# Optimization experiments

Hardware: AMD Instinct MI355X
Metric: run time of the kernel (lower is better)

Reference implementation:

```python
import jax, jax.numpy as jnp
import numpy as np

B, S, D, H = 32, 1024, 256, 256


def setup_inputs() -> dict:
    key = jax.random.key(0)
    ks = jax.random.split(key, 7)
    s_in = 1.0 / np.sqrt(D)
    s_h = 1.0 / np.sqrt(H)
    x = jax.random.normal(ks[0], (B, S, D), dtype=jnp.float32)
    # gate order: i, f, g, o stacked along last dim -> 4H
    W_fwd = jax.random.uniform(ks[1], (D, 4 * H), dtype=jnp.float32, minval=-s_in, maxval=s_in)
    U_fwd = jax.random.uniform(ks[2], (H, 4 * H), dtype=jnp.float32, minval=-s_h, maxval=s_h)
    b_fwd = jax.random.uniform(ks[3], (4 * H,), dtype=jnp.float32, minval=-s_in, maxval=s_in)
    W_rev = jax.random.uniform(ks[4], (D, 4 * H), dtype=jnp.float32, minval=-s_in, maxval=s_in)
    U_rev = jax.random.uniform(ks[5], (H, 4 * H), dtype=jnp.float32, minval=-s_h, maxval=s_h)
    b_rev = jax.random.uniform(ks[6], (4 * H,), dtype=jnp.float32, minval=-s_in, maxval=s_in)
    return {"x": x, "W_fwd": W_fwd, "U_fwd": U_fwd, "b_fwd": b_fwd,
            "W_rev": W_rev, "U_rev": U_rev, "b_rev": b_rev}


def _lstm_scan(x, W, U, b):
    # x: [B, S, D] -> outputs h over time: [B, S, H]
    hdim = U.shape[0]
    # precompute input projection for all steps: [S, B, 4H]
    xW = jnp.einsum('bsd,dg->sbg', x, W) + b

    def step(carry, xw_t):
        h, c = carry
        gates = xw_t + h @ U  # [B, 4H]
        i_t = jax.nn.sigmoid(gates[:, 0 * hdim:1 * hdim])
        f_t = jax.nn.sigmoid(gates[:, 1 * hdim:2 * hdim])
        g_t = jnp.tanh(gates[:, 2 * hdim:3 * hdim])
        o_t = jax.nn.sigmoid(gates[:, 3 * hdim:4 * hdim])
        c_t = f_t * c + i_t * g_t
        h_t = o_t * jnp.tanh(c_t)
        return (h_t, c_t), h_t

    bsz = x.shape[0]
    h0 = jnp.zeros((bsz, hdim), dtype=x.dtype)
    c0 = jnp.zeros((bsz, hdim), dtype=x.dtype)
    _, hs = jax.lax.scan(step, (h0, c0), xW)
    return jnp.transpose(hs, (1, 0, 2))  # [B, S, H]


def reference(x, W_fwd, U_fwd, b_fwd, W_rev, U_rev, b_rev):
    out_f = _lstm_scan(x, W_fwd, U_fwd, b_fwd)
    out_r = _lstm_scan(x[:, ::-1, :], W_rev, U_rev, b_rev)[:, ::-1, :]
    return jnp.concatenate([out_f, out_r], axis=2)  # [B, S, 2H]
```

## Files before the change

### kernel.cpp

```cpp
#include <hip/hip_runtime.h>
#include <hip/hip_bf16.h>

typedef _Float16 f16;
typedef _Float16 half8 __attribute__((ext_vector_type(8)));
typedef float f32x4 __attribute__((ext_vector_type(4)));


__global__ void prep_uq_kernel(const float* __restrict__ Uf, const float* __restrict__ Ur,
                               unsigned int* __restrict__ UQ, float* __restrict__ Uscale)
{
    int idx = blockIdx.x * 256 + threadIdx.x;
    if (idx >= 2048) return;
    int dir = idx >> 10, j = idx & 1023;
    const float* U = dir ? Ur : Uf;
    float m = 0.f;
    for (int k = 0; k < 256; ++k) m = fmaxf(m, fabsf(U[k * 1024 + j]));
    float sinv = (m > 0.f) ? 127.f / m : 0.f;
    for (int kk = 0; kk < 64; ++kk) {
        unsigned int w = 0;
        #pragma unroll
        for (int e = 0; e < 4; ++e) {
            float v = U[(kk * 4 + e) * 1024 + j];
            int q = __float2int_rn(v * sinv);
            w |= ((unsigned int)(q & 0xff)) << (8 * e);
        }
        UQ[(((size_t)dir * 16 + (kk >> 2)) * 1024 + j) * 4 + (kk & 3)] = w;
    }
    Uscale[idx] = m / (127.f * 127.f);
}

__global__ __launch_bounds__(256) void proj_gemm_kernel(
    const float* __restrict__ x, const float* __restrict__ Wf, const float* __restrict__ Wr,
    const float* __restrict__ bfw, const float* __restrict__ brw, f16* __restrict__ G)
{
    const int nt = blockIdx.x;
    const int mt = blockIdx.y;
    const int m0 = mt * 128, n0 = nt * 128;
    const int dir = n0 >> 10, nin0 = n0 & 1023;
    const float* W   = dir ? Wr : Wf;
    const float* bia = dir ? brw : bfw;
    __shared__ f16 Asm[128][40];
    __shared__ f16 Bsm[128][40];
    const int t = threadIdx.x;
    const int lane = t & 63, wave = t >> 6;
    const int wr = wave >> 1, wc = wave & 1;
    f32x4 acc[4][4] = {};
    for (int k0 = 0; k0 < 256; k0 += 32) {
        #pragma unroll
        for (int e = 0; e < 16; ++e) {
            int idx = e * 256 + t;
            int r = idx >> 5, kk = idx & 31;
            Asm[r][kk] = (f16)x[(size_t)(m0 + r) * 256 + (k0 + kk)];
        }
        #pragma unroll
        for (int e = 0; e < 16; ++e) {
            int idx = e * 256 + t;
            int col = idx & 127, kr = idx >> 7;
            Bsm[col][kr] = (f16)W[(size_t)(k0 + kr) * 1024 + (nin0 + col)];
        }
        __syncthreads();
        const int l15 = lane & 15, kb = (lane >> 4) * 8;
        half8 af[4], bfr[4];
        #pragma unroll
        for (int fr = 0; fr < 4; ++fr) af[fr]  = *(const half8*)&Asm[wr * 64 + fr * 16 + l15][kb];
        #pragma unroll
        for (int fc = 0; fc < 4; ++fc) bfr[fc] = *(const half8*)&Bsm[wc * 64 + fc * 16 + l15][kb];
        #pragma unroll
        for (int fr = 0; fr < 4; ++fr)
            #pragma unroll
            for (int fc = 0; fc < 4; ++fc)
                acc[fr][fc] = __builtin_amdgcn_mfma_f32_16x16x32_f16(af[fr], bfr[fc], acc[fr][fc], 0, 0, 0);
        __syncthreads();
    }
    const int row4 = (lane >> 4) * 4, c15 = lane & 15;
    #pragma unroll
    for (int fr = 0; fr < 4; ++fr)
        #pragma unroll
        for (int fc = 0; fc < 4; ++fc) {
            int rbase = m0 + wr * 64 + fr * 16 + row4;
            int cidx  = n0 + wc * 64 + fc * 16 + c15;
            float bv = bia[cidx & 1023];
            #pragma unroll
            for (int i = 0; i < 4; ++i)
                G[(size_t)(rbase + i) * 2048 + cidx] = (f16)(acc[fr][fc][i] + bv);
        }
}

__device__ __forceinline__ int dot4i8(unsigned int a, unsigned int b, int c) {
#if __has_builtin(__builtin_amdgcn_sdot4)
    return __builtin_amdgcn_sdot4(a, b, c, false);
#else
    c += (int)(signed char)(a)       * (int)(signed char)(b);
    c += (int)(signed char)(a >> 8)  * (int)(signed char)(b >> 8);
    c += (int)(signed char)(a >> 16) * (int)(signed char)(b >> 16);
    c += (int)(signed char)(a >> 24) * (int)(signed char)(b >> 24);
    return c;
#endif
}

__device__ __forceinline__ float tanh_fast(float x) {
    float e = __expf(2.f * x);
    return 1.f - 2.f / (e + 1.f);
}

__global__ __launch_bounds__(1024, 4) void scan_kernel(
    const f16* __restrict__ G, const unsigned int* __restrict__ UQ,
    const float* __restrict__ Uscale, float* __restrict__ out)
{
    const int wg = blockIdx.x;
    const int dir = wg >> 5, b = wg & 31;
    const int g = threadIdx.x;
    __shared__ __align__(16) unsigned int hq[64];
    __shared__ float preact[1024];

    uint4 ureg[16];
    #pragma unroll
    for (int kkk = 0; kkk < 16; ++kkk)
        ureg[kkk] = *(const uint4*)&UQ[(((size_t)dir * 16 + kkk) * 1024 + g) * 4];
    const float usc = Uscale[dir * 1024 + g];

    float c_state = 0.f;
    if (g < 64) hq[g] = 0u;
    const f16* Grow = G + (size_t)b * 1024 * 2048 + dir * 1024 + g;
    float* outp = out + (size_t)b * 1024 * 512 + dir * 256 + g;
    int s0 = dir ? 1023 : 0;
    f16 xw_c = Grow[(size_t)s0 * 2048];
    __syncthreads();

    for (int t = 0; t < 1024; ++t) {
        int tn = (t < 1023) ? (t + 1) : t;
        int sn = dir ? (1023 - tn) : tn;
        f16 xw_n = Grow[(size_t)sn * 2048];

        int i0 = 0, i1 = 0, i2 = 0, i3 = 0;
        #pragma unroll
        for (int kkk = 0; kkk < 16; ++kkk) {
            uint4 h4 = *(const uint4*)&hq[kkk * 4];
            i0 = dot4i8(ureg[kkk].x, h4.x, i0);
            i1 = dot4i8(ureg[kkk].y, h4.y, i1);
            i2 = dot4i8(ureg[kkk].z, h4.z, i2);
            i3 = dot4i8(ureg[kkk].w, h4.w, i3);
        }
        int iacc = (i0 + i1) + (i2 + i3);
        preact[g] = (float)xw_c + (float)iacc * usc;
        __syncthreads();

        if (g < 256) {
            float pi = preact[g];
            float pf = preact[256 + g];
            float pg = preact[512 + g];
            float po = preact[768 + g];
            float ig = 1.f / (1.f + __expf(-pi));
            float fg = 1.f / (1.f + __expf(-pf));
            float gg = tanh_fast(pg);
            float og = 1.f / (1.f + __expf(-po));
            c_state = fg * c_state + ig * gg;
            float h = og * tanh_fast(c_state);
            int s = dir ? (1023 - t) : t;
            outp[(size_t)s * 512] = h;
            int q = __float2int_rn(h * 127.f);
            ((signed char*)hq)[g] = (signed char)q;
        }
        __syncthreads();
        xw_c = xw_n;
    }
}

extern "C" void kernel_launch(void* const* d_in, const int* in_sizes, int n_in,
                              void* d_out, int out_size, void* d_ws, size_t ws_size,
                              hipStream_t stream) {
    const float* x  = (const float*)d_in[0];
    const float* Wf = (const float*)d_in[1];
    const float* Uf = (const float*)d_in[2];
    const float* bf = (const float*)d_in[3];
    const float* Wr = (const float*)d_in[4];
    const float* Ur = (const float*)d_in[5];
    const float* br = (const float*)d_in[6];
    float* out = (float*)d_out;

    char* ws = (char*)d_ws;
    unsigned int* UQ = (unsigned int*)ws;
    float* Uscale    = (float*)(ws + (size_t)512 * 1024);
    f16* G           = (f16*)(ws + (size_t)1024 * 1024);

    prep_uq_kernel<<<8, 256, 0, stream>>>(Uf, Ur, UQ, Uscale);
    dim3 gg(16, 256);
    proj_gemm_kernel<<<gg, 256, 0, stream>>>(x, Wf, Wr, bf, br, G);
    scan_kernel<<<64, 1024, 0, stream>>>(G, UQ, Uscale, out);
}
```

Before: 1.179 ms.

## Distribute quantized hidden state across lane quads and rotate via DPP

Instead of every thread reading all 64 words of the quantized hidden state from LDS each step, each lane in a quad loads a quarter (16 words) after the barrier. The quad then rotates these words with DPP moves three times so every lane sees all four quarters. The U weight registers are loaded in a lane-dependent rotated order to match. This cuts LDS broadcast reads to a quarter at the cost of 48 DPP moves per step and extra register pressure, with asm pins holding the weights in VGPRs.

```diff
diff --git a/kernel.cpp b/kernel.cpp
--- a/kernel.cpp
+++ b/kernel.cpp
@@ -98,10 +98,21 @@
 #endif
 }
 
+__device__ __forceinline__ int quad_rot1(int v) {
+#if __has_builtin(__builtin_amdgcn_mov_dpp)
+    return __builtin_amdgcn_mov_dpp(v, 0x39 , 0xF, 0xF, true);
+#else
+    int l = threadIdx.x & 63;
+    return __shfl(v, (l & ~3) | ((l + 1) & 3), 64);
+#endif
+}
+
 __device__ __forceinline__ float tanh_fast(float x) {
     float e = __expf(2.f * x);
     return 1.f - 2.f / (e + 1.f);
 }
+
+#define PIN4(u) asm volatile("" : "+v"(u.x), "+v"(u.y), "+v"(u.z), "+v"(u.w))
 
 __global__ __launch_bounds__(1024, 4) void scan_kernel(
     const f16* __restrict__ G, const unsigned int* __restrict__ UQ,
@@ -110,17 +121,28 @@
     const int wg = blockIdx.x;
     const int dir = wg >> 5, b = wg & 31;
     const int g = threadIdx.x;
+    const int q = g & 3;
     __shared__ __align__(16) unsigned int hq[64];
     __shared__ float preact[1024];
 
     uint4 ureg[16];
     #pragma unroll
-    for (int kkk = 0; kkk < 16; ++kkk)
-        ureg[kkk] = *(const uint4*)&UQ[(((size_t)dir * 16 + kkk) * 1024 + g) * 4];
+    for (int r = 0; r < 4; ++r) {
+        int p = (q + r) & 3;
+        #pragma unroll
+        for (int jj = 0; jj < 4; ++jj) {
+            int kkk = p * 4 + jj;
+            ureg[r * 4 + jj] = *(const uint4*)&UQ[(((size_t)dir * 16 + kkk) * 1024 + g) * 4];
+            PIN4(ureg[r * 4 + jj]);
+        }
+    }
     const float usc = Uscale[dir * 1024 + g];
 
+    int hd[16];
+    #pragma unroll
+    for (int m = 0; m < 16; ++m) hd[m] = 0;
+
     float c_state = 0.f;
-    if (g < 64) hq[g] = 0u;
     const f16* Grow = G + (size_t)b * 1024 * 2048 + dir * 1024 + g;
     float* outp = out + (size_t)b * 1024 * 512 + dir * 256 + g;
     int s0 = dir ? 1023 : 0;
@@ -134,12 +156,19 @@
 
         int i0 = 0, i1 = 0, i2 = 0, i3 = 0;
         #pragma unroll
-        for (int kkk = 0; kkk < 16; ++kkk) {
-            uint4 h4 = *(const uint4*)&hq[kkk * 4];
-            i0 = dot4i8(ureg[kkk].x, h4.x, i0);
-            i1 = dot4i8(ureg[kkk].y, h4.y, i1);
-            i2 = dot4i8(ureg[kkk].z, h4.z, i2);
-            i3 = dot4i8(ureg[kkk].w, h4.w, i3);
+        for (int r = 0; r < 4; ++r) {
+            #pragma unroll
+            for (int jj = 0; jj < 4; ++jj) {
+                const uint4 u = ureg[r * 4 + jj];
+                i0 = dot4i8(u.x, hd[jj * 4 + 0], i0);
+                i1 = dot4i8(u.y, hd[jj * 4 + 1], i1);
+                i2 = dot4i8(u.z, hd[jj * 4 + 2], i2);
+                i3 = dot4i8(u.w, hd[jj * 4 + 3], i3);
+            }
+            if (r < 3) {
+                #pragma unroll
+                for (int m = 0; m < 16; ++m) hd[m] = quad_rot1(hd[m]);
+            }
         }
         int iacc = (i0 + i1) + (i2 + i3);
         preact[g] = (float)xw_c + (float)iacc * usc;
@@ -158,10 +187,19 @@
             float h = og * tanh_fast(c_state);
             int s = dir ? (1023 - t) : t;
             outp[(size_t)s * 512] = h;
-            int q = __float2int_rn(h * 127.f);
-            ((signed char*)hq)[g] = (signed char)q;
-        }
-        __syncthreads();
+            int iq = __float2int_rn(h * 127.f);
+            ((signed char*)hq)[g] = (signed char)iq;
+        }
+        __syncthreads();
+
+        {
+            const uint4* hp = (const uint4*)((const char*)hq + q * 64);
+            uint4 a = hp[0], bq = hp[1], cq = hp[2], dq = hp[3];
+            hd[0] = a.x;  hd[1] = a.y;  hd[2] = a.z;  hd[3] = a.w;
+            hd[4] = bq.x; hd[5] = bq.y; hd[6] = bq.z; hd[7] = bq.w;
+            hd[8] = cq.x; hd[9] = cq.y; hd[10] = cq.z; hd[11] = cq.w;
+            hd[12] = dq.x; hd[13] = dq.y; hd[14] = dq.z; hd[15] = dq.w;
+        }
         xw_c = xw_n;
     }
 }
```

Result: slower. 1.408 ms (+19.5%).
